# Performance work log

Measured on AMD Instinct MI355X. Metric: run time of the kernel, lower is better.

The kernel has to match this reference:

```python
import jax, jax.numpy as jnp
import numpy as np

B_SZ = 4; L = 2048; IN_DIM = 32; D_MODEL = 256; N_LAYERS = 2
ED = 512; N_STATE = 16; DT_RANK = 16; D_CONV = 4


def setup_inputs() -> dict:
    key = jax.random.key(0)
    ks = jax.random.split(key, 12)
    def rn(k, shape, scale=0.02):
        return jax.random.normal(k, shape, jnp.float32) * scale
    return {
        "x": jax.random.normal(ks[0], (B_SZ, L, IN_DIM), jnp.float32),
        "enc_w": rn(ks[1], (D_MODEL, IN_DIM), 0.1),
        "enc_b": jnp.zeros((D_MODEL,), jnp.float32),
        "norm_w": jnp.ones((N_LAYERS, D_MODEL), jnp.float32),
        "in_proj_w": rn(ks[2], (N_LAYERS, 2 * ED, D_MODEL)),
        "conv_w": rn(ks[3], (N_LAYERS, ED, D_CONV), 0.1),
        "conv_b": jnp.zeros((N_LAYERS, ED), jnp.float32),
        "x_proj_w": rn(ks[4], (N_LAYERS, DT_RANK + 2 * N_STATE, ED)),
        "dt_proj_w": rn(ks[5], (N_LAYERS, ED, DT_RANK), 0.1),
        "dt_proj_b": rn(ks[6], (N_LAYERS, ED), 0.5),
        # S4D-real init: A_log[l, e, n] = log(n+1)
        "A_log": jnp.log(jnp.tile(jnp.arange(1, N_STATE + 1, dtype=jnp.float32), (N_LAYERS, ED, 1))),
        "D_param": jnp.ones((N_LAYERS, ED), jnp.float32),
        "out_proj_w": rn(ks[7], (N_LAYERS, D_MODEL, ED)),
        "dec_w": rn(ks[8], (1, D_MODEL), 0.1),
        "dec_b": jnp.zeros((1,), jnp.float32),
    }


def _rmsnorm(x, w, eps=1e-5):
    return x * jax.lax.rsqrt(jnp.mean(x * x, axis=-1, keepdims=True) + eps) * w


def _silu(x):
    return x * jax.nn.sigmoid(x)


def _selective_scan(x, delta, A, Bm, Cm, Dp):
    # x, delta: (B, L, ED); A: (ED, N); Bm, Cm: (B, L, N); Dp: (ED,)
    def step(h, t):
        d_t, b_t, c_t, x_t = t  # (B,ED) (B,N) (B,N) (B,ED)
        dA = jnp.exp(d_t[..., None] * A)               # (B, ED, N)
        h = dA * h + (d_t * x_t)[..., None] * b_t[:, None, :]
        y = jnp.einsum('ben,bn->be', h, c_t)
        return h, y
    h0 = jnp.zeros((x.shape[0], A.shape[0], A.shape[1]), x.dtype)
    xs = (jnp.swapaxes(delta, 0, 1), jnp.swapaxes(Bm, 0, 1),
          jnp.swapaxes(Cm, 0, 1), jnp.swapaxes(x, 0, 1))
    _, ys = jax.lax.scan(step, h0, xs)                 # ys: (L, B, ED)
    return jnp.swapaxes(ys, 0, 1) + Dp * x


def _mamba_block(x, p):
    xz = jnp.einsum('bld,ed->ble', x, p['in_proj_w'])  # (B, L, 2*ED)
    xb, z = jnp.split(xz, 2, axis=-1)
    # causal depthwise conv over time
    xc = jnp.swapaxes(xb, 1, 2)                        # (B, ED, L)
    kern = p['conv_w'][:, None, :]                     # (ED, 1, K)
    xc = jax.lax.conv_general_dilated(xc, kern, (1,), [(D_CONV - 1, 0)],
                                      feature_group_count=ED)
    xb = _silu(jnp.swapaxes(xc, 1, 2) + p['conv_b'])
    dbc = jnp.einsum('ble,fe->blf', xb, p['x_proj_w'])
    dt, Bm, Cm = jnp.split(dbc, [DT_RANK, DT_RANK + N_STATE], axis=-1)
    delta = jax.nn.softplus(jnp.einsum('blr,er->ble', dt, p['dt_proj_w']) + p['dt_proj_b'])
    A = -jnp.exp(p['A_log'])
    y = _selective_scan(xb, delta, A, Bm, Cm, p['D_param'])
    y = y * _silu(z)
    return jnp.einsum('ble,de->bld', y, p['out_proj_w'])


def reference(x, enc_w, enc_b, norm_w, in_proj_w, conv_w, conv_b, x_proj_w,
              dt_proj_w, dt_proj_b, A_log, D_param, out_proj_w, dec_w, dec_b):
    h = jnp.einsum('bli,di->bld', x, enc_w) + enc_b
    for l in range(N_LAYERS):
        p = {'in_proj_w': in_proj_w[l], 'conv_w': conv_w[l], 'conv_b': conv_b[l],
             'x_proj_w': x_proj_w[l], 'dt_proj_w': dt_proj_w[l], 'dt_proj_b': dt_proj_b[l],
             'A_log': A_log[l], 'D_param': D_param[l], 'out_proj_w': out_proj_w[l]}
        h = h + _mamba_block(_rmsnorm(h, norm_w[l]), p)
    out = jax.nn.sigmoid(jnp.einsum('bld,od->blo', h, dec_w) + dec_b)
    return out[:, -1, 0]
```

## Files before the change

kernel.cpp:

```cpp
#include <hip/hip_runtime.h>
#include <math.h>

#define BSZ 4
#define SEQ 2048
#define INDIM 32
#define DM 256
#define ED 512
#define NST 16
#define DTR 16
#define MROWS (BSZ * SEQ)
#define CH 64
#define LC (SEQ / CH)

typedef unsigned short u16;
typedef unsigned int u32;
typedef __bf16 bf16x8 __attribute__((ext_vector_type(8)));
typedef float f32x4 __attribute__((ext_vector_type(4)));

__device__ __forceinline__ float silu_f(float x) { return x / (1.f + __expf(-x)); }

__device__ __forceinline__ u16 f2bf(float x) {
  union { float f; unsigned u; } c; c.f = x;
  return (u16)((c.u + 0x7FFF + ((c.u >> 16) & 1)) >> 16);
}
__device__ __forceinline__ float bf2f(u16 v) {
  union { unsigned u; float f; } c; c.u = ((unsigned)v) << 16;
  return c.f;
}
__device__ __forceinline__ u32 pack2(float lo, float hi) {
  return (u32)f2bf(lo) | ((u32)f2bf(hi) << 16);
}

template <bool ACCUM>
__global__ __launch_bounds__(256) void gemm_bf16_f32(const u16* __restrict__ A,
                                                     const u16* __restrict__ B,
                                                     float* __restrict__ C,
                                                     int M, int N, int K,
                                                     int lda, int ldc) {
  __shared__ u16 As[128][40];
  __shared__ u16 Bs[128][40];
  const int tid = threadIdx.x;
  const int m0 = blockIdx.y * 128;
  const int n0 = blockIdx.x * 128;
  const int wid = tid >> 6;
  const int lane = tid & 63;
  const int wm = (wid >> 1) * 64, wn = (wid & 1) * 64;
  const int l15 = lane & 15, l4 = lane >> 4;
  const int arow = tid >> 1;
  const int ak = (tid & 1) * 16;
  f32x4 acc[4][4];
  const f32x4 zero = {0.f, 0.f, 0.f, 0.f};
#pragma unroll
  for (int i = 0; i < 4; i++)
#pragma unroll
    for (int j = 0; j < 4; j++) acc[i][j] = zero;

  for (int k0 = 0; k0 < K; k0 += 32) {
    const u16* ap = A + (size_t)(m0 + arow) * lda + k0 + ak;
    *(int4*)&As[arow][ak]     = *(const int4*)(ap);
    *(int4*)&As[arow][ak + 8] = *(const int4*)(ap + 8);
    int4 bv0 = {0, 0, 0, 0}, bv1 = {0, 0, 0, 0};
    if (n0 + arow < N) {
      const u16* bp = B + (size_t)(n0 + arow) * K + k0 + ak;
      bv0 = *(const int4*)(bp);
      bv1 = *(const int4*)(bp + 8);
    }
    *(int4*)&Bs[arow][ak]     = bv0;
    *(int4*)&Bs[arow][ak + 8] = bv1;
    __syncthreads();
    bf16x8 af[4], bfr[4];
#pragma unroll
    for (int i = 0; i < 4; i++) {
      af[i]  = *(const bf16x8*)&As[wm + i * 16 + l15][l4 * 8];
      bfr[i] = *(const bf16x8*)&Bs[wn + i * 16 + l15][l4 * 8];
    }
#pragma unroll
    for (int i = 0; i < 4; i++)
#pragma unroll
      for (int j = 0; j < 4; j++)
        acc[i][j] = __builtin_amdgcn_mfma_f32_16x16x32_bf16(af[i], bfr[j], acc[i][j], 0, 0, 0);
    __syncthreads();
  }
#pragma unroll
  for (int i = 0; i < 4; i++) {
    const int mb = m0 + wm + i * 16 + l4 * 4;
#pragma unroll
    for (int j = 0; j < 4; j++) {
      const int n = n0 + wn + j * 16 + l15;
      if (n < N) {
        float* p = C + (size_t)mb * ldc + n;
#pragma unroll
        for (int r = 0; r < 4; r++) {
          float v = acc[i][j][r];
          if (ACCUM) v += p[(size_t)r * ldc];
          p[(size_t)r * ldc] = v;
        }
      }
    }
  }
}

__global__ __launch_bounds__(256) void gemm_bf16_u16(const u16* __restrict__ A,
                                                     const u16* __restrict__ B,
                                                     u16* __restrict__ C,
                                                     int M, int N, int K,
                                                     int lda, int ldc) {
  __shared__ u16 As[128][40];
  __shared__ u16 Bs[128][40];
  const int tid = threadIdx.x;
  const int m0 = blockIdx.y * 128;
  const int n0 = blockIdx.x * 128;
  const int wid = tid >> 6;
  const int lane = tid & 63;
  const int wm = (wid >> 1) * 64, wn = (wid & 1) * 64;
  const int l15 = lane & 15, l4 = lane >> 4;
  const int arow = tid >> 1;
  const int ak = (tid & 1) * 16;
  f32x4 acc[4][4];
  const f32x4 zero = {0.f, 0.f, 0.f, 0.f};
#pragma unroll
  for (int i = 0; i < 4; i++)
#pragma unroll
    for (int j = 0; j < 4; j++) acc[i][j] = zero;

  for (int k0 = 0; k0 < K; k0 += 32) {
    const u16* ap = A + (size_t)(m0 + arow) * lda + k0 + ak;
    *(int4*)&As[arow][ak]     = *(const int4*)(ap);
    *(int4*)&As[arow][ak + 8] = *(const int4*)(ap + 8);
    const u16* bp = B + (size_t)(n0 + arow) * K + k0 + ak;
    *(int4*)&Bs[arow][ak]     = *(const int4*)(bp);
    *(int4*)&Bs[arow][ak + 8] = *(const int4*)(bp + 8);
    __syncthreads();
    bf16x8 af[4], bfr[4];
#pragma unroll
    for (int i = 0; i < 4; i++) {
      af[i]  = *(const bf16x8*)&As[wm + i * 16 + l15][l4 * 8];
      bfr[i] = *(const bf16x8*)&Bs[wn + i * 16 + l15][l4 * 8];
    }
#pragma unroll
    for (int i = 0; i < 4; i++)
#pragma unroll
      for (int j = 0; j < 4; j++)
        acc[i][j] = __builtin_amdgcn_mfma_f32_16x16x32_bf16(af[i], bfr[j], acc[i][j], 0, 0, 0);
    __syncthreads();
  }
#pragma unroll
  for (int i = 0; i < 4; i++) {
    const int mb = m0 + wm + i * 16 + l4 * 4;
#pragma unroll
    for (int j = 0; j < 4; j++) {
      const int n = n0 + wn + j * 16 + l15;
      u16* p = C + (size_t)mb * ldc + n;
#pragma unroll
      for (int r = 0; r < 4; r++) p[(size_t)r * ldc] = f2bf(acc[i][j][r]);
    }
  }
}

__global__ __launch_bounds__(256) void gemm_nt_enc(const float* __restrict__ A,
                                                   const float* __restrict__ B,
                                                   const float* __restrict__ bias,
                                                   float* __restrict__ C,
                                                   int M, int N, int K, int lda) {
  __shared__ float As[16][65];
  __shared__ float Bs[16][65];
  const int tid = threadIdx.x;
  const int m0 = blockIdx.y * 64;
  const int n0 = blockIdx.x * 64;
  const int tm = tid & 15, tn = tid >> 4;
  const int lrow = tid >> 2;
  const int lk = (tid & 3) << 2;
  float acc[4][4] = {};
  for (int k0 = 0; k0 < K; k0 += 16) {
    {
      const float4 a = *(const float4*)(A + (size_t)(m0 + lrow) * lda + k0 + lk);
      As[lk + 0][lrow] = a.x; As[lk + 1][lrow] = a.y;
      As[lk + 2][lrow] = a.z; As[lk + 3][lrow] = a.w;
    }
    {
      float4 b = make_float4(0.f, 0.f, 0.f, 0.f);
      if (n0 + lrow < N) b = *(const float4*)(B + (size_t)(n0 + lrow) * K + k0 + lk);
      Bs[lk + 0][lrow] = b.x; Bs[lk + 1][lrow] = b.y;
      Bs[lk + 2][lrow] = b.z; Bs[lk + 3][lrow] = b.w;
    }
    __syncthreads();
#pragma unroll
    for (int k = 0; k < 16; k++) {
      float a4[4], b4[4];
#pragma unroll
      for (int i = 0; i < 4; i++) a4[i] = As[k][tm * 4 + i];
#pragma unroll
      for (int j = 0; j < 4; j++) b4[j] = Bs[k][tn * 4 + j];
#pragma unroll
      for (int i = 0; i < 4; i++)
#pragma unroll
        for (int j = 0; j < 4; j++) acc[i][j] = fmaf(a4[i], b4[j], acc[i][j]);
    }
    __syncthreads();
  }
#pragma unroll
  for (int i = 0; i < 4; i++) {
    const int m = m0 + tm * 4 + i;
#pragma unroll
    for (int j = 0; j < 4; j++) {
      const int n = n0 + tn * 4 + j;
      if (n < N) C[(size_t)m * N + n] = acc[i][j] + bias[n];
    }
  }
}

#define S_IN (2 * 1024 * 256)
#define S_OUT (2 * 256 * 512)
#define S_XP (2 * 48 * 512)
__global__ __launch_bounds__(256) void cvt_weights_k(const float* __restrict__ w1,
                                                     const float* __restrict__ w2,
                                                     const float* __restrict__ w3,
                                                     u16* __restrict__ o1,
                                                     u16* __restrict__ o2,
                                                     u16* __restrict__ o3) {
  const int i = blockIdx.x * 256 + threadIdx.x;
  if (i < S_IN) o1[i] = f2bf(w1[i]);
  else if (i < S_IN + S_OUT) o2[i - S_IN] = f2bf(w2[i - S_IN]);
  else if (i < S_IN + S_OUT + S_XP) o3[i - S_IN - S_OUT] = f2bf(w3[i - S_IN - S_OUT]);
}

__global__ __launch_bounds__(256) void rmsnorm_k(const float* __restrict__ h,
                                                 const float* __restrict__ w,
                                                 u16* __restrict__ out16) {
  __shared__ float sh[4];
  __shared__ float sscale;
  const int row = blockIdx.x;
  const int tid = threadIdx.x;
  const float v = h[(size_t)row * DM + tid];
  float s = v * v;
#pragma unroll
  for (int off = 32; off; off >>= 1) s += __shfl_xor(s, off, 64);
  if ((tid & 63) == 0) sh[tid >> 6] = s;
  __syncthreads();
  if (tid == 0) {
    float t = sh[0] + sh[1] + sh[2] + sh[3];
    sscale = rsqrtf(t * (1.0f / DM) + 1e-5f);
  }
  __syncthreads();
  out16[(size_t)row * DM + tid] = f2bf(v * sscale * w[tid]);
}

__global__ __launch_bounds__(256) void conv_silu_k(const u16* __restrict__ xz16,
                                                   const float* __restrict__ cw,
                                                   const float* __restrict__ cb,
                                                   u16* __restrict__ out16) {
  const int idx = blockIdx.x * 256 + threadIdx.x;
  const int e = idx & (ED - 1);
  const int row = idx >> 9;
  const int t = row & (SEQ - 1);
  const float4 w = *(const float4*)(cw + e * 4);
  const u16* col = xz16 + e;
  float acc = cb[e];
  const float v0 = (t >= 3) ? bf2f(col[(size_t)(row - 3) * 1024]) : 0.f;
  const float v1 = (t >= 2) ? bf2f(col[(size_t)(row - 2) * 1024]) : 0.f;
  const float v2 = (t >= 1) ? bf2f(col[(size_t)(row - 1) * 1024]) : 0.f;
  const float v3 = bf2f(col[(size_t)row * 1024]);
  acc += v0 * w.x + v1 * w.y + v2 * w.z + v3 * w.w;
  out16[idx] = f2bf(silu_f(acc));
}

__global__ __launch_bounds__(256) void dt_softplus_k(const float* __restrict__ dbc,
                                                     const float* __restrict__ dtw,
                                                     const float* __restrict__ dtb,
                                                     const u16* __restrict__ xbc16,
                                                     u32* __restrict__ pairs) {
  __shared__ float sdt[DTR];
  const int row = blockIdx.y;
  const int e = blockIdx.x * 256 + threadIdx.x;
  if (threadIdx.x < DTR) sdt[threadIdx.x] = dbc[(size_t)row * 48 + threadIdx.x];
  __syncthreads();
  const float* w = dtw + (size_t)e * DTR;
  float s = dtb[e];
#pragma unroll
  for (int r = 0; r < DTR; r++) s = fmaf(sdt[r], w[r], s);
  const float sp = fmaxf(s, 0.f) + log1pf(__expf(-fabsf(s)));
  const float xv = bf2f(xbc16[(size_t)row * ED + e]);
  pairs[(size_t)row * ED + e] = pack2(sp, sp * xv);
}

__global__ __launch_bounds__(256) void scan_pass1(const u32* __restrict__ pairs,
                                                  const float* __restrict__ dbc,
                                                  u16* __restrict__ hend16,
                                                  float* __restrict__ Sbuf,
                                                  const float* __restrict__ A_log) {
  __shared__ float sB[LC][16];
  const int tid = threadIdx.x;
  const int e = blockIdx.x * 256 + tid;
  const int c = blockIdx.y;
  const int b = blockIdx.z;
  const int row0 = b * SEQ + c * LC;
  float Aen[16];
  {
    const float4* ap = (const float4*)(A_log + (size_t)e * 16);
#pragma unroll
    for (int q = 0; q < 4; q++) {
      float4 v = ap[q];
      Aen[4 * q + 0] = -__expf(v.x); Aen[4 * q + 1] = -__expf(v.y);
      Aen[4 * q + 2] = -__expf(v.z); Aen[4 * q + 3] = -__expf(v.w);
    }
  }
  for (int idx = tid; idx < LC * 16; idx += 256)
    sB[idx >> 4][idx & 15] = dbc[(size_t)(row0 + (idx >> 4)) * 48 + DTR + (idx & 15)];
  __syncthreads();
  const u32* pp = pairs + (size_t)row0 * ED + e;
  float h[16];
#pragma unroll
  for (int n = 0; n < 16; n++) h[n] = 0.f;
  float S = 0.f;
  u32 p = pp[0];
  for (int t = 0; t < LC; t++) {
    const u32 pn = (t + 1 < LC) ? pp[(size_t)(t + 1) * ED] : p;
    const float d = bf2f((u16)(p & 0xffff));
    const float dx = bf2f((u16)(p >> 16));
    S += d;
    const float4* bp = (const float4*)sB[t];
    const float4 B0 = bp[0], B1 = bp[1], B2 = bp[2], B3 = bp[3];
    const float Bv[16] = {B0.x, B0.y, B0.z, B0.w, B1.x, B1.y, B1.z, B1.w,
                          B2.x, B2.y, B2.z, B2.w, B3.x, B3.y, B3.z, B3.w};
#pragma unroll
    for (int n = 0; n < 16; n++) h[n] = __expf(d * Aen[n]) * h[n] + dx * Bv[n];
    p = pn;
  }
  u32 wbuf[8];
#pragma unroll
  for (int q = 0; q < 8; q++) wbuf[q] = pack2(h[2 * q], h[2 * q + 1]);
  u16* hp = hend16 + ((size_t)(c * BSZ + b) * ED + e) * 16;
  *(int4*)(hp) = *(int4*)&wbuf[0];
  *(int4*)(hp + 8) = *(int4*)&wbuf[4];
  Sbuf[(size_t)(c * BSZ + b) * ED + e] = S;
}

__global__ __launch_bounds__(256) void scan_mid(u16* __restrict__ hend16,
                                                const float* __restrict__ Sbuf,
                                                const float* __restrict__ A_log) {
  const int idx = blockIdx.x * 256 + threadIdx.x;
  const int en = idx & 8191;
  const int b = idx >> 13;
  const int e = en >> 4;
  const float A = -__expf(A_log[en]);
  float h = 0.f;
#pragma unroll 4
  for (int c = 0; c < CH; c++) {
    const size_t base = (size_t)(c * BSZ + b) * 8192 + en;
    const float he = bf2f(hend16[base]);
    const float Sv = Sbuf[(size_t)(c * BSZ + b) * ED + e];
    hend16[base] = f2bf(h);
    h = __expf(A * Sv) * h + he;
  }
}

__global__ __launch_bounds__(256) void scan_pass2(const u32* __restrict__ pairs,
                                                  const u16* __restrict__ xbc16,
                                                  const float* __restrict__ dbc,
                                                  u16* __restrict__ xz16,
                                                  const u16* __restrict__ hin16,
                                                  const float* __restrict__ A_log,
                                                  const float* __restrict__ Dp) {
  __shared__ float sB[LC][16];
  __shared__ float sC[LC][16];
  const int tid = threadIdx.x;
  const int e = blockIdx.x * 256 + tid;
  const int c = blockIdx.y;
  const int b = blockIdx.z;
  const int row0 = b * SEQ + c * LC;
  float Aen[16];
  {
    const float4* ap = (const float4*)(A_log + (size_t)e * 16);
#pragma unroll
    for (int q = 0; q < 4; q++) {
      float4 v = ap[q];
      Aen[4 * q + 0] = -__expf(v.x); Aen[4 * q + 1] = -__expf(v.y);
      Aen[4 * q + 2] = -__expf(v.z); Aen[4 * q + 3] = -__expf(v.w);
    }
  }
  for (int idx = tid; idx < LC * 32; idx += 256) {
    const int i = idx >> 5, jj = idx & 31;
    const float v = dbc[(size_t)(row0 + i) * 48 + DTR + jj];
    if (jj < 16) sB[i][jj] = v; else sC[i][jj - 16] = v;
  }
  __syncthreads();
  float h[16];
  {
    const u16* hp = hin16 + ((size_t)(c * BSZ + b) * ED + e) * 16;
    int4 v0 = *(const int4*)(hp);
    int4 v1 = *(const int4*)(hp + 8);
    const u32* wv = (const u32*)&v0;
    const u32* wv1 = (const u32*)&v1;
#pragma unroll
    for (int q = 0; q < 4; q++) {
      h[2 * q] = bf2f((u16)(wv[q] & 0xffff));
      h[2 * q + 1] = bf2f((u16)(wv[q] >> 16));
      h[8 + 2 * q] = bf2f((u16)(wv1[q] & 0xffff));
      h[8 + 2 * q + 1] = bf2f((u16)(wv1[q] >> 16));
    }
  }
  const float De = Dp[e];
  const u32* pp = pairs + (size_t)row0 * ED + e;
  const u16* xp = xbc16 + (size_t)row0 * ED + e;
  const u16* zp = xz16 + (size_t)row0 * 1024 + ED + e;
  u16* yw = xz16 + (size_t)row0 * 1024 + e;
  u32 p = pp[0];
  float xv = bf2f(xp[0]);
  float zv = bf2f(zp[0]);
  for (int t = 0; t < LC; t++) {
    const int tn = (t + 1 < LC) ? t + 1 : t;
    const u32 pn = pp[(size_t)tn * ED];
    const float xnx = bf2f(xp[(size_t)tn * ED]);
    const float znx = bf2f(zp[(size_t)tn * 1024]);
    const float d = bf2f((u16)(p & 0xffff));
    const float dx = bf2f((u16)(p >> 16));
    const float4* bp = (const float4*)sB[t];
    const float4 B0 = bp[0], B1 = bp[1], B2 = bp[2], B3 = bp[3];
    const float Bv[16] = {B0.x, B0.y, B0.z, B0.w, B1.x, B1.y, B1.z, B1.w,
                          B2.x, B2.y, B2.z, B2.w, B3.x, B3.y, B3.z, B3.w};
    const float4* cp = (const float4*)sC[t];
    const float4 C0 = cp[0], C1 = cp[1], C2 = cp[2], C3 = cp[3];
    const float Cv[16] = {C0.x, C0.y, C0.z, C0.w, C1.x, C1.y, C1.z, C1.w,
                          C2.x, C2.y, C2.z, C2.w, C3.x, C3.y, C3.z, C3.w};
    float y0 = 0.f, y1 = 0.f, y2 = 0.f, y3 = 0.f;
#pragma unroll
    for (int n = 0; n < 16; n++) {
      h[n] = __expf(d * Aen[n]) * h[n] + dx * Bv[n];
      if ((n & 3) == 0) y0 = fmaf(h[n], Cv[n], y0);
      else if ((n & 3) == 1) y1 = fmaf(h[n], Cv[n], y1);
      else if ((n & 3) == 2) y2 = fmaf(h[n], Cv[n], y2);
      else y3 = fmaf(h[n], Cv[n], y3);
    }
    float y = ((y0 + y1) + (y2 + y3)) + De * xv;
    y *= silu_f(zv);
    yw[(size_t)t * 1024] = f2bf(y);
    p = pn; xv = xnx; zv = znx;
  }
}

__global__ __launch_bounds__(64) void decode_k(const float* __restrict__ h,
                                               const float* __restrict__ dw,
                                               const float* __restrict__ db,
                                               float* __restrict__ out) {
  const int b = blockIdx.x;
  const int tid = threadIdx.x;
  const float* row = h + ((size_t)b * SEQ + SEQ - 1) * DM;
  float s = 0.f;
  for (int i = tid; i < DM; i += 64) s = fmaf(row[i], dw[i], s);
#pragma unroll
  for (int off = 32; off; off >>= 1) s += __shfl_xor(s, off, 64);
  if (tid == 0) out[b] = 1.f / (1.f + __expf(-(s + db[0])));
}

extern "C" void kernel_launch(void* const* d_in, const int* in_sizes, int n_in,
                              void* d_out, int out_size, void* d_ws, size_t ws_size,
                              hipStream_t stream) {
  const float* x         = (const float*)d_in[0];
  const float* enc_w     = (const float*)d_in[1];
  const float* enc_b     = (const float*)d_in[2];
  const float* norm_w    = (const float*)d_in[3];
  const float* in_proj_w = (const float*)d_in[4];
  const float* conv_w    = (const float*)d_in[5];
  const float* conv_b    = (const float*)d_in[6];
  const float* x_proj_w  = (const float*)d_in[7];
  const float* dt_proj_w = (const float*)d_in[8];
  const float* dt_proj_b = (const float*)d_in[9];
  const float* A_log     = (const float*)d_in[10];
  const float* D_param   = (const float*)d_in[11];
  const float* out_proj_w= (const float*)d_in[12];
  const float* dec_w     = (const float*)d_in[13];
  const float* dec_b     = (const float*)d_in[14];
  float* out = (float*)d_out;

  float* ws = (float*)d_ws;
  float* h       = ws;
  u16*   xz16    = (u16*)(ws + 2097152);
  u16*   xbc16   = (u16*)(ws + 6291456);
  u32*   pairs   = (u32*)(ws + 8388608);
  float* dbc     = ws + 12582912;
  u16*   hend16  = (u16*)(ws + 12976128);
  float* Sbuf    = ws + 14024704;
  u16*   w16in   = (u16*)(ws + 14155776);
  u16*   w16out  = (u16*)(ws + 14417920);
  u16*   w16xp   = (u16*)(ws + 14548992);
  u16*   normed16 = hend16;

  const dim3 blk(256);

  cvt_weights_k<<<(S_IN + S_OUT + S_XP + 255) / 256, blk, 0, stream>>>(
      in_proj_w, out_proj_w, x_proj_w, w16in, w16out, w16xp);

  gemm_nt_enc<<<dim3(DM / 64, MROWS / 64), blk, 0, stream>>>(
      x, enc_w, enc_b, h, MROWS, DM, INDIM, INDIM);

  for (int l = 0; l < 2; l++) {
    const float* Al = A_log + (size_t)l * ED * NST;
    rmsnorm_k<<<MROWS, 256, 0, stream>>>(h, norm_w + (size_t)l * DM, normed16);
    gemm_bf16_u16<<<dim3(1024 / 128, MROWS / 128), blk, 0, stream>>>(
        normed16, w16in + (size_t)l * 1024 * DM, xz16, MROWS, 1024, DM, DM, 1024);
    conv_silu_k<<<(MROWS * ED) / 256, blk, 0, stream>>>(
        xz16, conv_w + (size_t)l * ED * 4, conv_b + (size_t)l * ED, xbc16);
    gemm_bf16_f32<false><<<dim3(1, MROWS / 128), blk, 0, stream>>>(
        xbc16, w16xp + (size_t)l * 48 * ED, dbc, MROWS, 48, ED, ED, 48);
    dt_softplus_k<<<dim3(2, MROWS), blk, 0, stream>>>(
        dbc, dt_proj_w + (size_t)l * ED * DTR, dt_proj_b + (size_t)l * ED,
        xbc16, pairs);
    scan_pass1<<<dim3(ED / 256, CH, BSZ), blk, 0, stream>>>(
        pairs, dbc, hend16, Sbuf, Al);
    scan_mid<<<(BSZ * ED * NST) / 256, blk, 0, stream>>>(hend16, Sbuf, Al);
    scan_pass2<<<dim3(ED / 256, CH, BSZ), blk, 0, stream>>>(
        pairs, xbc16, dbc, xz16, hend16, Al, D_param + (size_t)l * ED);
    gemm_bf16_f32<true><<<dim3(DM / 128, MROWS / 128), blk, 0, stream>>>(
        xz16, w16out + (size_t)l * DM * ED, h, MROWS, DM, ED, 1024, DM);
  }

  decode_k<<<4, 64, 0, stream>>>(h, dec_w, dec_b, out);
}
```

Baseline: 394.8 us.

## Fold dt_proj into x_proj GEMM and fuse out_proj with residual, rmsnorm, decode

Precomputes a combined x_proj·dt_proj weight so one GEMM produces delta directly. Softplus and the (delta, delta*x) pair packing move into that GEMM's epilogue, replacing the separate dt_softplus kernel. The out_proj GEMM becomes a row-panel kernel that adds the residual and then either applies the next layer's RMSNorm or computes the final sigmoid decode, removing the standalone rmsnorm and decode launches. The cost is more FLOPs in the x_proj GEMM (N grows from 48 to 544), lower precision from rounding the combined weight to bf16, and extra weight-prep work on every call.

```diff
diff --git a/kernel.cpp b/kernel.cpp
--- a/kernel.cpp
+++ b/kernel.cpp
@@ -11,6 +11,7 @@
 #define MROWS (BSZ * SEQ)
 #define CH 64
 #define LC (SEQ / CH)
+#define WXPE_LSTRIDE (544 * 512)
 
 typedef unsigned short u16;
 typedef unsigned int u32;
@@ -31,10 +32,9 @@
   return (u32)f2bf(lo) | ((u32)f2bf(hi) << 16);
 }
 
-template <bool ACCUM>
-__global__ __launch_bounds__(256) void gemm_bf16_f32(const u16* __restrict__ A,
+__global__ __launch_bounds__(256) void gemm_bf16_u16(const u16* __restrict__ A,
                                                      const u16* __restrict__ B,
-                                                     float* __restrict__ C,
+                                                     u16* __restrict__ C,
                                                      int M, int N, int K,
                                                      int lda, int ldc) {
   __shared__ u16 As[128][40];
@@ -59,14 +59,9 @@
     const u16* ap = A + (size_t)(m0 + arow) * lda + k0 + ak;
     *(int4*)&As[arow][ak]     = *(const int4*)(ap);
     *(int4*)&As[arow][ak + 8] = *(const int4*)(ap + 8);
-    int4 bv0 = {0, 0, 0, 0}, bv1 = {0, 0, 0, 0};
-    if (n0 + arow < N) {
-      const u16* bp = B + (size_t)(n0 + arow) * K + k0 + ak;
-      bv0 = *(const int4*)(bp);
-      bv1 = *(const int4*)(bp + 8);
-    }
-    *(int4*)&Bs[arow][ak]     = bv0;
-    *(int4*)&Bs[arow][ak + 8] = bv1;
+    const u16* bp = B + (size_t)(n0 + arow) * K + k0 + ak;
+    *(int4*)&Bs[arow][ak]     = *(const int4*)(bp);
+    *(int4*)&Bs[arow][ak + 8] = *(const int4*)(bp + 8);
     __syncthreads();
     bf16x8 af[4], bfr[4];
 #pragma unroll
@@ -87,24 +82,18 @@
 #pragma unroll
     for (int j = 0; j < 4; j++) {
       const int n = n0 + wn + j * 16 + l15;
-      if (n < N) {
-        float* p = C + (size_t)mb * ldc + n;
-#pragma unroll
-        for (int r = 0; r < 4; r++) {
-          float v = acc[i][j][r];
-          if (ACCUM) v += p[(size_t)r * ldc];
-          p[(size_t)r * ldc] = v;
-        }
-      }
-    }
-  }
-}
-
-__global__ __launch_bounds__(256) void gemm_bf16_u16(const u16* __restrict__ A,
-                                                     const u16* __restrict__ B,
-                                                     u16* __restrict__ C,
-                                                     int M, int N, int K,
-                                                     int lda, int ldc) {
+      u16* p = C + (size_t)mb * ldc + n;
+#pragma unroll
+      for (int r = 0; r < 4; r++) p[(size_t)r * ldc] = f2bf(acc[i][j][r]);
+    }
+  }
+}
+
+__global__ __launch_bounds__(256) void gemm_xproj(const u16* __restrict__ A,
+                                                  const u16* __restrict__ Bw,
+                                                  const float* __restrict__ dtb,
+                                                  u32* __restrict__ pairs,
+                                                  float* __restrict__ BCout) {
   __shared__ u16 As[128][40];
   __shared__ u16 Bs[128][40];
   const int tid = threadIdx.x;
@@ -123,13 +112,18 @@
 #pragma unroll
     for (int j = 0; j < 4; j++) acc[i][j] = zero;
 
-  for (int k0 = 0; k0 < K; k0 += 32) {
-    const u16* ap = A + (size_t)(m0 + arow) * lda + k0 + ak;
+  for (int k0 = 0; k0 < ED; k0 += 32) {
+    const u16* ap = A + (size_t)(m0 + arow) * ED + k0 + ak;
     *(int4*)&As[arow][ak]     = *(const int4*)(ap);
     *(int4*)&As[arow][ak + 8] = *(const int4*)(ap + 8);
-    const u16* bp = B + (size_t)(n0 + arow) * K + k0 + ak;
-    *(int4*)&Bs[arow][ak]     = *(const int4*)(bp);
-    *(int4*)&Bs[arow][ak + 8] = *(const int4*)(bp + 8);
+    int4 bv0 = {0, 0, 0, 0}, bv1 = {0, 0, 0, 0};
+    if (n0 + arow < 544) {
+      const u16* bp = Bw + (size_t)(n0 + arow) * ED + k0 + ak;
+      bv0 = *(const int4*)(bp);
+      bv1 = *(const int4*)(bp + 8);
+    }
+    *(int4*)&Bs[arow][ak]     = bv0;
+    *(int4*)&Bs[arow][ak + 8] = bv1;
     __syncthreads();
     bf16x8 af[4], bfr[4];
 #pragma unroll
@@ -150,9 +144,100 @@
 #pragma unroll
     for (int j = 0; j < 4; j++) {
       const int n = n0 + wn + j * 16 + l15;
-      u16* p = C + (size_t)mb * ldc + n;
-#pragma unroll
-      for (int r = 0; r < 4; r++) p[(size_t)r * ldc] = f2bf(acc[i][j][r]);
+      if (n < 512) {
+        const float bias = dtb[n];
+#pragma unroll
+        for (int r = 0; r < 4; r++) {
+          const int row = mb + r;
+          const float v = acc[i][j][r] + bias;
+          const float sp = fmaxf(v, 0.f) + log1pf(__expf(-fabsf(v)));
+          const float xv = bf2f(A[(size_t)row * ED + n]);
+          pairs[(size_t)row * ED + n] = pack2(sp, sp * xv);
+        }
+      } else if (n < 544) {
+#pragma unroll
+        for (int r = 0; r < 4; r++)
+          BCout[(size_t)(mb + r) * 32 + (n - 512)] = acc[i][j][r];
+      }
+    }
+  }
+}
+
+template <bool NORM, bool DECODE>
+__global__ __launch_bounds__(256) void outproj_fused(const u16* __restrict__ A,
+                                                     const u16* __restrict__ Bw,
+                                                     float* __restrict__ hio,
+                                                     u16* __restrict__ normed16,
+                                                     const float* __restrict__ norm_w,
+                                                     const float* __restrict__ dec_w,
+                                                     const float* __restrict__ dec_b,
+                                                     float* __restrict__ out) {
+  __shared__ u16 As[64][40];
+  __shared__ u16 Bs[256][40];
+  const int tid = threadIdx.x;
+  const int m0 = blockIdx.x * 64;
+  const int wid = tid >> 6;
+  const int lane = tid & 63;
+  const int l15 = lane & 15, l4 = lane >> 4;
+  f32x4 acc[16];
+  const f32x4 zero = {0.f, 0.f, 0.f, 0.f};
+#pragma unroll
+  for (int j = 0; j < 16; j++) acc[j] = zero;
+  const int arow = tid >> 2, ac = (tid & 3) * 8;
+
+  for (int k0 = 0; k0 < 512; k0 += 32) {
+    *(int4*)&As[arow][ac] = *(const int4*)(A + (size_t)(m0 + arow) * 1024 + k0 + ac);
+#pragma unroll
+    for (int q = 0; q < 4; q++)
+      *(int4*)&Bs[tid][q * 8] = *(const int4*)(Bw + (size_t)tid * 512 + k0 + q * 8);
+    __syncthreads();
+    const bf16x8 af = *(const bf16x8*)&As[16 * wid + l15][l4 * 8];
+#pragma unroll
+    for (int j = 0; j < 16; j++) {
+      const bf16x8 bfr = *(const bf16x8*)&Bs[16 * j + l15][l4 * 8];
+      acc[j] = __builtin_amdgcn_mfma_f32_16x16x32_bf16(af, bfr, acc[j], 0, 0, 0);
+    }
+    __syncthreads();
+  }
+  float nw[16], dw[16];
+  if (NORM) {
+#pragma unroll
+    for (int j = 0; j < 16; j++) nw[j] = norm_w[16 * j + l15];
+  }
+  if (DECODE) {
+#pragma unroll
+    for (int j = 0; j < 16; j++) dw[j] = dec_w[16 * j + l15];
+  }
+  const int rbase = m0 + 16 * wid + l4 * 4;
+#pragma unroll
+  for (int r = 0; r < 4; r++) {
+    const int row = rbase + r;
+    float* hp = hio + (size_t)row * 256;
+    float v[16];
+#pragma unroll
+    for (int j = 0; j < 16; j++) v[j] = acc[j][r] + hp[16 * j + l15];
+#pragma unroll
+    for (int j = 0; j < 16; j++) hp[16 * j + l15] = v[j];
+    if (NORM) {
+      float s = 0.f;
+#pragma unroll
+      for (int j = 0; j < 16; j++) s = fmaf(v[j], v[j], s);
+      s += __shfl_xor(s, 1); s += __shfl_xor(s, 2);
+      s += __shfl_xor(s, 4); s += __shfl_xor(s, 8);
+      const float sc = rsqrtf(s * (1.0f / 256.0f) + 1e-5f);
+#pragma unroll
+      for (int j = 0; j < 16; j++)
+        normed16[(size_t)row * 256 + 16 * j + l15] = f2bf(v[j] * sc * nw[j]);
+    }
+    if (DECODE) {
+      if ((row & (SEQ - 1)) == SEQ - 1) {
+        float p = 0.f;
+#pragma unroll
+        for (int j = 0; j < 16; j++) p = fmaf(v[j], dw[j], p);
+        p += __shfl_xor(p, 1); p += __shfl_xor(p, 2);
+        p += __shfl_xor(p, 4); p += __shfl_xor(p, 8);
+        if (l15 == 0) out[row >> 11] = 1.f / (1.f + __expf(-(p + dec_b[0])));
+      }
     }
   }
 }
@@ -211,17 +296,39 @@
 
 #define S_IN (2 * 1024 * 256)
 #define S_OUT (2 * 256 * 512)
-#define S_XP (2 * 48 * 512)
-__global__ __launch_bounds__(256) void cvt_weights_k(const float* __restrict__ w1,
-                                                     const float* __restrict__ w2,
-                                                     const float* __restrict__ w3,
-                                                     u16* __restrict__ o1,
-                                                     u16* __restrict__ o2,
-                                                     u16* __restrict__ o3) {
+#define S_BC (2 * 32 * 512)
+#define S_WC (2 * 512 * 512)
+__global__ __launch_bounds__(256) void prep_k(const float* __restrict__ w1,
+                                              const float* __restrict__ w2,
+                                              const float* __restrict__ xpw,
+                                              const float* __restrict__ dtw,
+                                              u16* __restrict__ o1,
+                                              u16* __restrict__ o2,
+                                              u16* __restrict__ wxpe) {
   const int i = blockIdx.x * 256 + threadIdx.x;
-  if (i < S_IN) o1[i] = f2bf(w1[i]);
-  else if (i < S_IN + S_OUT) o2[i - S_IN] = f2bf(w2[i - S_IN]);
-  else if (i < S_IN + S_OUT + S_XP) o3[i - S_IN - S_OUT] = f2bf(w3[i - S_IN - S_OUT]);
+  if (i < S_IN) {
+    o1[i] = f2bf(w1[i]);
+  } else if (i < S_IN + S_OUT) {
+    o2[i - S_IN] = f2bf(w2[i - S_IN]);
+  } else if (i < S_IN + S_OUT + S_BC) {
+    const int i2 = i - S_IN - S_OUT;
+    const int l = i2 >> 14;
+    const int r = (i2 >> 9) & 31;
+    const int k = i2 & 511;
+    wxpe[(size_t)l * WXPE_LSTRIDE + (512 + r) * 512 + k] =
+        f2bf(xpw[(size_t)l * 48 * 512 + (16 + r) * 512 + k]);
+  } else if (i < S_IN + S_OUT + S_BC + S_WC) {
+    const int i2 = i - S_IN - S_OUT - S_BC;
+    const int l = i2 >> 18;
+    const int e = (i2 >> 9) & 511;
+    const int k = i2 & 511;
+    const float* dwp = dtw + ((size_t)l * 512 + e) * 16;
+    const float* xw = xpw + (size_t)l * 48 * 512 + k;
+    float s = 0.f;
+#pragma unroll
+    for (int r = 0; r < 16; r++) s = fmaf(dwp[r], xw[(size_t)r * 512], s);
+    wxpe[(size_t)l * WXPE_LSTRIDE + (size_t)e * 512 + k] = f2bf(s);
+  }
 }
 
 __global__ __launch_bounds__(256) void rmsnorm_k(const float* __restrict__ h,
@@ -264,27 +371,8 @@
   out16[idx] = f2bf(silu_f(acc));
 }
 
-__global__ __launch_bounds__(256) void dt_softplus_k(const float* __restrict__ dbc,
-                                                     const float* __restrict__ dtw,
-                                                     const float* __restrict__ dtb,
-                                                     const u16* __restrict__ xbc16,
-                                                     u32* __restrict__ pairs) {
-  __shared__ float sdt[DTR];
-  const int row = blockIdx.y;
-  const int e = blockIdx.x * 256 + threadIdx.x;
-  if (threadIdx.x < DTR) sdt[threadIdx.x] = dbc[(size_t)row * 48 + threadIdx.x];
-  __syncthreads();
-  const float* w = dtw + (size_t)e * DTR;
-  float s = dtb[e];
-#pragma unroll
-  for (int r = 0; r < DTR; r++) s = fmaf(sdt[r], w[r], s);
-  const float sp = fmaxf(s, 0.f) + log1pf(__expf(-fabsf(s)));
-  const float xv = bf2f(xbc16[(size_t)row * ED + e]);
-  pairs[(size_t)row * ED + e] = pack2(sp, sp * xv);
-}
-
 __global__ __launch_bounds__(256) void scan_pass1(const u32* __restrict__ pairs,
-                                                  const float* __restrict__ dbc,
+                                                  const float* __restrict__ BC,
                                                   u16* __restrict__ hend16,
                                                   float* __restrict__ Sbuf,
                                                   const float* __restrict__ A_log) {
@@ -305,7 +393,7 @@
     }
   }
   for (int idx = tid; idx < LC * 16; idx += 256)
-    sB[idx >> 4][idx & 15] = dbc[(size_t)(row0 + (idx >> 4)) * 48 + DTR + (idx & 15)];
+    sB[idx >> 4][idx & 15] = BC[(size_t)(row0 + (idx >> 4)) * 32 + (idx & 15)];
   __syncthreads();
   const u32* pp = pairs + (size_t)row0 * ED + e;
   float h[16];
@@ -356,7 +444,7 @@
 
 __global__ __launch_bounds__(256) void scan_pass2(const u32* __restrict__ pairs,
                                                   const u16* __restrict__ xbc16,
-                                                  const float* __restrict__ dbc,
+                                                  const float* __restrict__ BC,
                                                   u16* __restrict__ xz16,
                                                   const u16* __restrict__ hin16,
                                                   const float* __restrict__ A_log,
@@ -380,7 +468,7 @@
   }
   for (int idx = tid; idx < LC * 32; idx += 256) {
     const int i = idx >> 5, jj = idx & 31;
-    const float v = dbc[(size_t)(row0 + i) * 48 + DTR + jj];
+    const float v = BC[(size_t)(row0 + i) * 32 + jj];
     if (jj < 16) sB[i][jj] = v; else sC[i][jj - 16] = v;
   }
   __syncthreads();
@@ -438,20 +526,6 @@
   }
 }
 
-__global__ __launch_bounds__(64) void decode_k(const float* __restrict__ h,
-                                               const float* __restrict__ dw,
-                                               const float* __restrict__ db,
-                                               float* __restrict__ out) {
-  const int b = blockIdx.x;
-  const int tid = threadIdx.x;
-  const float* row = h + ((size_t)b * SEQ + SEQ - 1) * DM;
-  float s = 0.f;
-  for (int i = tid; i < DM; i += 64) s = fmaf(row[i], dw[i], s);
-#pragma unroll
-  for (int off = 32; off; off >>= 1) s += __shfl_xor(s, off, 64);
-  if (tid == 0) out[b] = 1.f / (1.f + __expf(-(s + db[0])));
-}
-
 extern "C" void kernel_launch(void* const* d_in, const int* in_sizes, int n_in,
                               void* d_out, int out_size, void* d_ws, size_t ws_size,
                               hipStream_t stream) {
@@ -477,42 +551,44 @@
   u16*   xz16    = (u16*)(ws + 2097152);
   u16*   xbc16   = (u16*)(ws + 6291456);
   u32*   pairs   = (u32*)(ws + 8388608);
-  float* dbc     = ws + 12582912;
-  u16*   hend16  = (u16*)(ws + 12976128);
-  float* Sbuf    = ws + 14024704;
-  u16*   w16in   = (u16*)(ws + 14155776);
-  u16*   w16out  = (u16*)(ws + 14417920);
-  u16*   w16xp   = (u16*)(ws + 14548992);
-  u16*   normed16 = hend16;
+  float* BC      = ws + 12582912;
+  u16*   hbuf    = (u16*)(ws + 12845056);
+  float* Sbuf    = ws + 13893632;
+  u16*   w16in   = (u16*)(ws + 14024704);
+  u16*   w16out  = (u16*)(ws + 14286848);
+  u16*   wxpe    = (u16*)(ws + 14417920);
+  u16*   normed16 = hbuf;
 
   const dim3 blk(256);
 
-  cvt_weights_k<<<(S_IN + S_OUT + S_XP + 255) / 256, blk, 0, stream>>>(
-      in_proj_w, out_proj_w, x_proj_w, w16in, w16out, w16xp);
+  prep_k<<<(S_IN + S_OUT + S_BC + S_WC + 255) / 256, blk, 0, stream>>>(
+      in_proj_w, out_proj_w, x_proj_w, dt_proj_w, w16in, w16out, wxpe);
 
   gemm_nt_enc<<<dim3(DM / 64, MROWS / 64), blk, 0, stream>>>(
       x, enc_w, enc_b, h, MROWS, DM, INDIM, INDIM);
+  rmsnorm_k<<<MROWS, 256, 0, stream>>>(h, norm_w, normed16);
 
   for (int l = 0; l < 2; l++) {
     const float* Al = A_log + (size_t)l * ED * NST;
-    rmsnorm_k<<<MROWS, 256, 0, stream>>>(h, norm_w + (size_t)l * DM, normed16);
+    const float* Dl = D_param + (size_t)l * ED;
     gemm_bf16_u16<<<dim3(1024 / 128, MROWS / 128), blk, 0, stream>>>(
         normed16, w16in + (size_t)l * 1024 * DM, xz16, MROWS, 1024, DM, DM, 1024);
     conv_silu_k<<<(MROWS * ED) / 256, blk, 0, stream>>>(
         xz16, conv_w + (size_t)l * ED * 4, conv_b + (size_t)l * ED, xbc16);
-    gemm_bf16_f32<false><<<dim3(1, MROWS / 128), blk, 0, stream>>>(
-        xbc16, w16xp + (size_t)l * 48 * ED, dbc, MROWS, 48, ED, ED, 48);
-    dt_softplus_k<<<dim3(2, MROWS), blk, 0, stream>>>(
-        dbc, dt_proj_w + (size_t)l * ED * DTR, dt_proj_b + (size_t)l * ED,
-        xbc16, pairs);
+    gemm_xproj<<<dim3(5, MROWS / 128), blk, 0, stream>>>(
+        xbc16, wxpe + (size_t)l * WXPE_LSTRIDE, dt_proj_b + (size_t)l * ED,
+        pairs, BC);
     scan_pass1<<<dim3(ED / 256, CH, BSZ), blk, 0, stream>>>(
-        pairs, dbc, hend16, Sbuf, Al);
-    scan_mid<<<(BSZ * ED * NST) / 256, blk, 0, stream>>>(hend16, Sbuf, Al);
+        pairs, BC, hbuf, Sbuf, Al);
+    scan_mid<<<(BSZ * ED * NST) / 256, blk, 0, stream>>>(hbuf, Sbuf, Al);
     scan_pass2<<<dim3(ED / 256, CH, BSZ), blk, 0, stream>>>(
-        pairs, xbc16, dbc, xz16, hend16, Al, D_param + (size_t)l * ED);
-    gemm_bf16_f32<true><<<dim3(DM / 128, MROWS / 128), blk, 0, stream>>>(
-        xz16, w16out + (size_t)l * DM * ED, h, MROWS, DM, ED, 1024, DM);
-  }
-
-  decode_k<<<4, 64, 0, stream>>>(h, dec_w, dec_b, out);
-}
+        pairs, xbc16, BC, xz16, hbuf, Al, Dl);
+    if (l == 0) {
+      outproj_fused<true, false><<<MROWS / 64, blk, 0, stream>>>(
+          xz16, w16out, h, normed16, norm_w + DM, nullptr, nullptr, nullptr);
+    } else {
+      outproj_fused<false, true><<<MROWS / 64, blk, 0, stream>>>(
+          xz16, w16out + (size_t)DM * ED, h, nullptr, nullptr, dec_w, dec_b, out);
+    }
+  }
+}
```

Result: no change. 394.8 us (-0.0%).
